# Performance work log

Hardware: AMD Instinct MI355X
Metric: run time of the kernel (lower is better)

## Reference

```python
import jax, jax.numpy as jnp
import numpy as np

N, D = 8192, 128

def setup_inputs() -> dict:
    key = jax.random.key(0)
    kF, kS = jax.random.split(key)
    F = jax.random.normal(kF, (N, D), dtype=jnp.float32)
    S = jax.random.uniform(kS, (N, N), dtype=jnp.float32)
    return {"F": F, "S": S, "t": 1, "T": 10}

def reference(F, S, t, T):
    # Pairwise squared euclidean distances via Gram trick:
    # D_ij = ||f_i||^2 + ||f_j||^2 - 2 f_i . f_j  (same math as norm(F[:,None]-F)^2)
    sq = jnp.sum(F * F, axis=1)                      # [N]
    dist2 = sq[:, None] + sq[None, :] - 2.0 * (F @ F.T)  # [N, N]
    # select=False: loss = sum over i of sum_j dist2[i,j] * S[i,j]
    loss = jnp.sum(dist2 * S)
    return loss
```

## Files before the change

### kernel.cpp

```cpp
#include <hip/hip_runtime.h>

#define NN 8192
#define DD 128
#define BM 128
#define NTILE (NN / BM)

typedef __attribute__((ext_vector_type(8))) short bf16x8;
typedef __attribute__((ext_vector_type(4))) float f32x4;

__device__ __forceinline__ ushort f2bf(float x) {
    unsigned u = __float_as_uint(x);
    unsigned r = u + 0x7FFFu + ((u >> 16) & 1u);
    return (ushort)(r >> 16);
}

__global__ void sq_kernel(const float* __restrict__ F, float* __restrict__ sq) {
    int gtid = blockIdx.x * blockDim.x + threadIdx.x;
    int row  = gtid >> 6;
    int lane = threadIdx.x & 63;
    const float2 v = *(const float2*)(F + (size_t)row * DD + lane * 2);
    float s = v.x * v.x + v.y * v.y;
    #pragma unroll
    for (int off = 32; off > 0; off >>= 1) s += __shfl_down(s, off);
    if (lane == 0) sq[row] = s;
}

__global__ __launch_bounds__(256, 2) void tile_kernel(
        const float* __restrict__ F, const float* __restrict__ S,
        const float* __restrict__ sq, float* __restrict__ partials) {
    __shared__ ushort lA[BM * DD];
    __shared__ ushort lB[BM * DD];
    __shared__ float  sqi[BM];
    __shared__ float  sqj[BM];
    __shared__ float  red[4];

    const int bi = blockIdx.y, bj = blockIdx.x;
    const int gi = bi * BM, gj = bj * BM;
    const int tid = threadIdx.x;

    {
        const int r0 = tid >> 5;
        const int c4 = (tid & 31) * 4;
        #pragma unroll
        for (int it = 0; it < 16; ++it) {
            const int row = it * 8 + r0;
            const float4 va = *(const float4*)(F + (size_t)(gi + row) * DD + c4);
            const float4 vb = *(const float4*)(F + (size_t)(gj + row) * DD + c4);
            int byte = row * 256 + c4 * 2;
            byte ^= (row & 7) << 4;
            *(ushort4*)((char*)lA + byte) =
                make_ushort4(f2bf(va.x), f2bf(va.y), f2bf(va.z), f2bf(va.w));
            *(ushort4*)((char*)lB + byte) =
                make_ushort4(f2bf(vb.x), f2bf(vb.y), f2bf(vb.z), f2bf(vb.w));
        }
        if (tid < 128) sqi[tid] = sq[gi + tid];
        else           sqj[tid - 128] = sq[gj + tid - 128];
    }
    __syncthreads();

    const int w  = tid >> 6;
    const int l  = tid & 63;
    const int fr = l & 15;
    const int g  = l >> 4;
    const int wr = w * 32;

    bf16x8 afrag[2][4];
    #pragma unroll
    for (int mt = 0; mt < 2; ++mt)
        #pragma unroll
        for (int kk = 0; kk < 4; ++kk) {
            const int row = wr + mt * 16 + fr;
            int byte = row * 256 + (kk * 32 + g * 8) * 2;
            byte ^= (row & 7) << 4;
            afrag[mt][kk] = *(const bf16x8*)((const char*)lA + byte);
        }

    f32x4 acc[2][8];
    #pragma unroll
    for (int mt = 0; mt < 2; ++mt)
        #pragma unroll
        for (int nt = 0; nt < 8; ++nt) acc[mt][nt] = (f32x4){0.f, 0.f, 0.f, 0.f};

    #pragma unroll
    for (int nt = 0; nt < 8; ++nt) {
        #pragma unroll
        for (int kk = 0; kk < 4; ++kk) {
            const int row = nt * 16 + fr;
            int byte = row * 256 + (kk * 32 + g * 8) * 2;
            byte ^= (row & 7) << 4;
            const bf16x8 bfrag = *(const bf16x8*)((const char*)lB + byte);
            acc[0][nt] = __builtin_amdgcn_mfma_f32_16x16x32_bf16(
                afrag[0][kk], bfrag, acc[0][nt], 0, 0, 0);
            acc[1][nt] = __builtin_amdgcn_mfma_f32_16x16x32_bf16(
                afrag[1][kk], bfrag, acc[1][nt], 0, 0, 0);
        }
    }

    float part = 0.f;
    float sj[8];
    #pragma unroll
    for (int nt = 0; nt < 8; ++nt) sj[nt] = sqj[nt * 16 + fr];

    #pragma unroll
    for (int mt = 0; mt < 2; ++mt) {
        #pragma unroll
        for (int r = 0; r < 4; ++r) {
            const int rowt = wr + mt * 16 + g * 4 + r;
            const float si = sqi[rowt];
            const float* srow = S + (size_t)(gi + rowt) * NN + gj + fr;
            #pragma unroll
            for (int nt = 0; nt < 8; ++nt) {
                const float s = srow[nt * 16];
                part += s * (si + sj[nt] - 2.0f * acc[mt][nt][r]);
            }
        }
    }

    #pragma unroll
    for (int off = 32; off > 0; off >>= 1) part += __shfl_down(part, off);
    if (l == 0) red[w] = part;
    __syncthreads();
    if (tid == 0)
        partials[blockIdx.y * gridDim.x + blockIdx.x] = (red[0] + red[1]) + (red[2] + red[3]);
}

__global__ void reduce_kernel(const float* __restrict__ partials, float* __restrict__ out) {
    __shared__ float sm[256];
    const int t = threadIdx.x;
    float s = 0.f;
    for (int i = t; i < NTILE * NTILE; i += 256) s += partials[i];
    sm[t] = s;
    __syncthreads();
    for (int off = 128; off > 0; off >>= 1) {
        if (t < off) sm[t] += sm[t + off];
        __syncthreads();
    }
    if (t == 0) out[0] = sm[0];
}

extern "C" void kernel_launch(void* const* d_in, const int* in_sizes, int n_in,
                              void* d_out, int out_size, void* d_ws, size_t ws_size,
                              hipStream_t stream) {
    const float* F = (const float*)d_in[0];
    const float* S = (const float*)d_in[1];
    float* ws       = (float*)d_ws;
    float* sq       = ws;
    float* partials = ws + NN;
    float* out      = (float*)d_out;

    sq_kernel<<<NN / 4, 256, 0, stream>>>(F, sq);
    dim3 grid(NTILE, NTILE);
    tile_kernel<<<grid, 256, 0, stream>>>(F, S, sq, partials);
    reduce_kernel<<<1, 256, 0, stream>>>(partials, out);
}
```

Before: 77.58 us.

## Pre-convert F to bf16, async-load tiles to LDS, vectorize and prefetch S loads

The prep kernel now also writes a bf16 copy of F to workspace. When the workspace is large enough, the tile kernel fills LDS directly with async global-to-LDS loads instead of loading fp32 and converting in every block. The wave-to-tile mapping is also swapped so each lane reads contiguous float4 runs of S, issued before the MFMA loop so the S traffic overlaps compute. This adds an extra global write of bf16 F, and falls back to the old path if the workspace is too small.

```diff
diff --git a/kernel.cpp b/kernel.cpp
--- a/kernel.cpp
+++ b/kernel.cpp
@@ -14,22 +14,38 @@
     return (ushort)(r >> 16);
 }
 
-__global__ void sq_kernel(const float* __restrict__ F, float* __restrict__ sq) {
+__device__ __forceinline__ void async16(void* lds, const void* g) {
+    __builtin_amdgcn_global_load_lds(
+        (const __attribute__((address_space(1))) unsigned*)g,
+        (__attribute__((address_space(3))) unsigned*)lds, 16, 0, 0);
+}
+__device__ __forceinline__ void async4(void* lds, const void* g) {
+    __builtin_amdgcn_global_load_lds(
+        (const __attribute__((address_space(1))) unsigned*)g,
+        (__attribute__((address_space(3))) unsigned*)lds, 4, 0, 0);
+}
+
+__global__ void prep_kernel(const float* __restrict__ F, ushort* __restrict__ Fbf,
+                            float* __restrict__ sq, int doFbf) {
     int gtid = blockIdx.x * blockDim.x + threadIdx.x;
     int row  = gtid >> 6;
     int lane = threadIdx.x & 63;
     const float2 v = *(const float2*)(F + (size_t)row * DD + lane * 2);
+    if (doFbf)
+        ((ushort2*)(Fbf + (size_t)row * DD))[lane] = make_ushort2(f2bf(v.x), f2bf(v.y));
     float s = v.x * v.x + v.y * v.y;
     #pragma unroll
     for (int off = 32; off > 0; off >>= 1) s += __shfl_down(s, off);
     if (lane == 0) sq[row] = s;
 }
 
+template <int FAST>
 __global__ __launch_bounds__(256, 2) void tile_kernel(
-        const float* __restrict__ F, const float* __restrict__ S,
-        const float* __restrict__ sq, float* __restrict__ partials) {
-    __shared__ ushort lA[BM * DD];
-    __shared__ ushort lB[BM * DD];
+        const ushort* __restrict__ Fbf, const float* __restrict__ F,
+        const float* __restrict__ S, const float* __restrict__ sq,
+        float* __restrict__ partials) {
+    __shared__ ushort lI[BM * DD];
+    __shared__ ushort lJ[BM * DD];
     __shared__ float  sqi[BM];
     __shared__ float  sqj[BM];
     __shared__ float  red[4];
@@ -37,8 +53,24 @@
     const int bi = blockIdx.y, bj = blockIdx.x;
     const int gi = bi * BM, gj = bj * BM;
     const int tid = threadIdx.x;
-
-    {
+    const int w = tid >> 6, l = tid & 63;
+
+    if (FAST) {
+        #pragma unroll
+        for (int it = 0; it < 8; ++it) {
+            const int chunk = it * 4 + w;
+            const int row = chunk * 4 + (l >> 4);
+            const int inb = (l & 15) * 16;
+            const int src = inb ^ ((row & 7) << 4);
+            async16((char*)lI + chunk * 1024, (const char*)(Fbf + (size_t)(gi + row) * DD) + src);
+            async16((char*)lJ + chunk * 1024, (const char*)(Fbf + (size_t)(gj + row) * DD) + src);
+        }
+        {
+            float* dstb = (w < 2 ? sqi : sqj) + (w & 1) * 64;
+            const float* srcb = sq + (w < 2 ? gi : gj) + (w & 1) * 64 + l;
+            async4(dstb, srcb);
+        }
+    } else {
         const int r0 = tid >> 5;
         const int c4 = (tid & 31) * 4;
         #pragma unroll
@@ -48,9 +80,9 @@
             const float4 vb = *(const float4*)(F + (size_t)(gj + row) * DD + c4);
             int byte = row * 256 + c4 * 2;
             byte ^= (row & 7) << 4;
-            *(ushort4*)((char*)lA + byte) =
+            *(ushort4*)((char*)lI + byte) =
                 make_ushort4(f2bf(va.x), f2bf(va.y), f2bf(va.z), f2bf(va.w));
-            *(ushort4*)((char*)lB + byte) =
+            *(ushort4*)((char*)lJ + byte) =
                 make_ushort4(f2bf(vb.x), f2bf(vb.y), f2bf(vb.z), f2bf(vb.w));
         }
         if (tid < 128) sqi[tid] = sq[gi + tid];
@@ -58,62 +90,72 @@
     }
     __syncthreads();
 
-    const int w  = tid >> 6;
-    const int l  = tid & 63;
     const int fr = l & 15;
     const int g  = l >> 4;
-    const int wr = w * 32;
+    const int jw = w * 32;
+
+    float4 sv0[8], sv1[8];
+    #pragma unroll
+    for (int ct = 0; ct < 8; ++ct) {
+        const float* srow = S + (size_t)(gi + ct * 16 + fr) * NN + gj + jw + g * 4;
+        sv0[ct] = *(const float4*)(srow);
+        sv1[ct] = *(const float4*)(srow + 16);
+    }
 
     bf16x8 afrag[2][4];
     #pragma unroll
-    for (int mt = 0; mt < 2; ++mt)
+    for (int kk = 0; kk < 4; ++kk) {
+        {
+            const int row = jw + fr;
+            int byte = row * 256 + kk * 64 + g * 16;
+            byte ^= (row & 7) << 4;
+            afrag[0][kk] = *(const bf16x8*)((const char*)lJ + byte);
+        }
+        {
+            const int row = jw + 16 + fr;
+            int byte = row * 256 + kk * 64 + g * 16;
+            byte ^= (row & 7) << 4;
+            afrag[1][kk] = *(const bf16x8*)((const char*)lJ + byte);
+        }
+    }
+
+    f32x4 acc[2][8];
+    #pragma unroll
+    for (int ct = 0; ct < 8; ++ct) {
+        acc[0][ct] = (f32x4){0.f, 0.f, 0.f, 0.f};
+        acc[1][ct] = (f32x4){0.f, 0.f, 0.f, 0.f};
+    }
+
+    #pragma unroll
+    for (int ct = 0; ct < 8; ++ct) {
         #pragma unroll
         for (int kk = 0; kk < 4; ++kk) {
-            const int row = wr + mt * 16 + fr;
-            int byte = row * 256 + (kk * 32 + g * 8) * 2;
-            byte ^= (row & 7) << 4;
-            afrag[mt][kk] = *(const bf16x8*)((const char*)lA + byte);
-        }
-
-    f32x4 acc[2][8];
-    #pragma unroll
-    for (int mt = 0; mt < 2; ++mt)
-        #pragma unroll
-        for (int nt = 0; nt < 8; ++nt) acc[mt][nt] = (f32x4){0.f, 0.f, 0.f, 0.f};
-
-    #pragma unroll
-    for (int nt = 0; nt < 8; ++nt) {
-        #pragma unroll
-        for (int kk = 0; kk < 4; ++kk) {
-            const int row = nt * 16 + fr;
-            int byte = row * 256 + (kk * 32 + g * 8) * 2;
-            byte ^= (row & 7) << 4;
-            const bf16x8 bfrag = *(const bf16x8*)((const char*)lB + byte);
-            acc[0][nt] = __builtin_amdgcn_mfma_f32_16x16x32_bf16(
-                afrag[0][kk], bfrag, acc[0][nt], 0, 0, 0);
-            acc[1][nt] = __builtin_amdgcn_mfma_f32_16x16x32_bf16(
-                afrag[1][kk], bfrag, acc[1][nt], 0, 0, 0);
-        }
-    }
-
+            const int row = ct * 16 + fr;
+            int byte = row * 256 + kk * 64 + g * 16;
+            byte ^= (row & 7) << 4;
+            const bf16x8 bfrag = *(const bf16x8*)((const char*)lI + byte);
+            acc[0][ct] = __builtin_amdgcn_mfma_f32_16x16x32_bf16(
+                afrag[0][kk], bfrag, acc[0][ct], 0, 0, 0);
+            acc[1][ct] = __builtin_amdgcn_mfma_f32_16x16x32_bf16(
+                afrag[1][kk], bfrag, acc[1][ct], 0, 0, 0);
+        }
+    }
+
+    const float4 sj0 = *(const float4*)(sqj + jw + g * 4);
+    const float4 sj1 = *(const float4*)(sqj + jw + 16 + g * 4);
     float part = 0.f;
-    float sj[8];
-    #pragma unroll
-    for (int nt = 0; nt < 8; ++nt) sj[nt] = sqj[nt * 16 + fr];
-
-    #pragma unroll
-    for (int mt = 0; mt < 2; ++mt) {
-        #pragma unroll
-        for (int r = 0; r < 4; ++r) {
-            const int rowt = wr + mt * 16 + g * 4 + r;
-            const float si = sqi[rowt];
-            const float* srow = S + (size_t)(gi + rowt) * NN + gj + fr;
-            #pragma unroll
-            for (int nt = 0; nt < 8; ++nt) {
-                const float s = srow[nt * 16];
-                part += s * (si + sj[nt] - 2.0f * acc[mt][nt][r]);
-            }
-        }
+    #pragma unroll
+    for (int ct = 0; ct < 8; ++ct) {
+        const float si = sqi[ct * 16 + fr];
+        const float4 s0 = sv0[ct], s1 = sv1[ct];
+        part += s0.x * (si + sj0.x - 2.f * acc[0][ct][0]);
+        part += s0.y * (si + sj0.y - 2.f * acc[0][ct][1]);
+        part += s0.z * (si + sj0.z - 2.f * acc[0][ct][2]);
+        part += s0.w * (si + sj0.w - 2.f * acc[0][ct][3]);
+        part += s1.x * (si + sj1.x - 2.f * acc[1][ct][0]);
+        part += s1.y * (si + sj1.y - 2.f * acc[1][ct][1]);
+        part += s1.z * (si + sj1.z - 2.f * acc[1][ct][2]);
+        part += s1.w * (si + sj1.w - 2.f * acc[1][ct][3]);
     }
 
     #pragma unroll
@@ -143,13 +185,19 @@
                               hipStream_t stream) {
     const float* F = (const float*)d_in[0];
     const float* S = (const float*)d_in[1];
-    float* ws       = (float*)d_ws;
-    float* sq       = ws;
-    float* partials = ws + NN;
+    float* sq       = (float*)d_ws;
+    float* partials = sq + NN;
+    ushort* Fbf     = (ushort*)((char*)d_ws + 48 * 1024);
     float* out      = (float*)d_out;
 
-    sq_kernel<<<NN / 4, 256, 0, stream>>>(F, sq);
+    const size_t need = 48 * 1024 + (size_t)NN * DD * 2 + 256;
+    const int fast = (ws_size >= need) ? 1 : 0;
+
+    prep_kernel<<<NN / 4, 256, 0, stream>>>(F, Fbf, sq, fast);
     dim3 grid(NTILE, NTILE);
-    tile_kernel<<<grid, 256, 0, stream>>>(F, S, sq, partials);
+    if (fast)
+        tile_kernel<1><<<grid, 256, 0, stream>>>(Fbf, F, S, sq, partials);
+    else
+        tile_kernel<0><<<grid, 256, 0, stream>>>(Fbf, F, S, sq, partials);
     reduce_kernel<<<1, 256, 0, stream>>>(partials, out);
 }
```

After: 69.13 us. -10.9%, faster.
